# Kernel tuning notes

Measured on AMD Instinct MI355X. Metric: run time of the kernel, lower is better.

The kernel has to match this reference:

```python
import jax, jax.numpy as jnp
import numpy as np

N_NODES = 100000
N_EDGES = 600000
F_IN = 128
F_OUT = 128


def setup_inputs() -> dict:
    key = jax.random.key(0)
    ks = jax.random.split(key, 9)
    stdv = 1.0 / np.sqrt(F_OUT)
    return {
        "x": jax.random.normal(ks[0], (N_NODES, F_IN), dtype=jnp.float32),
        "weight": jax.random.uniform(ks[1], (F_IN, F_OUT), dtype=jnp.float32, minval=-stdv, maxval=stdv),
        "bias": jax.random.uniform(ks[2], (F_OUT,), dtype=jnp.float32, minval=-stdv, maxval=stdv),
        "vals0": jax.random.uniform(ks[3], (N_EDGES,), dtype=jnp.float32),
        "vals1": jax.random.uniform(ks[4], (N_EDGES,), dtype=jnp.float32),
        "rows0": jax.random.randint(ks[5], (N_EDGES,), 0, N_NODES, dtype=jnp.int32),
        "cols0": jax.random.randint(ks[6], (N_EDGES,), 0, N_NODES, dtype=jnp.int32),
        "rows1": jax.random.randint(ks[7], (N_EDGES,), 0, N_NODES, dtype=jnp.int32),
        "cols1": jax.random.randint(ks[8], (N_EDGES,), 0, N_NODES, dtype=jnp.int32),
    }


def _spmm(rows, cols, vals, dense, n):
    # COO sparse [n,n] @ dense [n,f]: gather source rows, scale, scatter-add to dest rows
    msgs = dense[cols] * vals[:, None]          # [E, f]
    return jax.ops.segment_sum(msgs, rows, num_segments=n)


def reference(x, weight, bias, vals0, vals1, rows0, cols0, rows1, cols1):
    n = x.shape[0]
    support = x @ weight                         # [N, F_OUT] dense GEMM
    out = _spmm(rows0, cols0, vals0, support, n) \
        + _spmm(rows1, cols1, vals1, support, n)
    return out + bias
```

## Files before the change

kernel.cpp:

```cpp
#include <hip/hip_runtime.h>


#define FDIM 128
#define EPB 2048

typedef __attribute__((ext_vector_type(8))) short short8;
typedef __attribute__((ext_vector_type(4))) float floatx4;

__device__ __forceinline__ unsigned short f32_to_bf16(float f) {
    unsigned int u = __float_as_uint(f);
    unsigned int r = u + 0x7fffu + ((u >> 16) & 1u);
    return (unsigned short)(r >> 16);
}

__device__ __forceinline__ float bf16_lo(unsigned int u) {
    return __uint_as_float((u & 0xffffu) << 16);
}
__device__ __forceinline__ float bf16_hi(unsigned int u) {
    return __uint_as_float(u & 0xffff0000u);
}

__global__ __launch_bounds__(256) void wt_conv(const float* __restrict__ w,
                                               unsigned short* __restrict__ wt) {
    int idx = blockIdx.x * 256 + threadIdx.x;
    int nn = idx >> 7, k = idx & 127;
    wt[idx] = f32_to_bf16(w[(size_t)k * FDIM + nn]);
}

__global__ __launch_bounds__(256) void gemm_mfma(const float* __restrict__ x,
                                                 const unsigned short* __restrict__ wt,
                                                 unsigned short* __restrict__ support,
                                                 int n) {
    __shared__ __align__(16) short As[64][136];
    __shared__ __align__(16) short Bs[128][136];
    const int tid = threadIdx.x;
    const int m0 = blockIdx.x * 64;

    #pragma unroll
    for (int i = 0; i < 8; ++i) {
        int idx = tid + i * 256;
        int r = idx >> 5, c4 = idx & 31;
        float4 v = make_float4(0.f, 0.f, 0.f, 0.f);
        if (m0 + r < n) v = *(const float4*)(x + (size_t)(m0 + r) * FDIM + c4 * 4);
        short4 s;
        s.x = (short)f32_to_bf16(v.x); s.y = (short)f32_to_bf16(v.y);
        s.z = (short)f32_to_bf16(v.z); s.w = (short)f32_to_bf16(v.w);
        *(short4*)&As[r][c4 * 4] = s;
    }
    #pragma unroll
    for (int i = 0; i < 8; ++i) {
        int idx = tid + i * 256;
        int r = idx >> 4, c8 = idx & 15;
        short8 v = *(const short8*)(wt + (size_t)r * FDIM + c8 * 8);
        *(short8*)&Bs[r][c8 * 8] = v;
    }
    __syncthreads();

    const int wv = tid >> 6;
    const int lane = tid & 63;
    const int quad = lane >> 4;
    const int lr = lane & 15;

    floatx4 acc[8];
    #pragma unroll
    for (int nt = 0; nt < 8; ++nt) acc[nt] = (floatx4)0.f;

    #pragma unroll
    for (int ks = 0; ks < 4; ++ks) {
        short8 a = *(const short8*)&As[wv * 16 + lr][ks * 32 + quad * 8];
        #pragma unroll
        for (int nt = 0; nt < 8; ++nt) {
            short8 b = *(const short8*)&Bs[nt * 16 + lr][ks * 32 + quad * 8];
            acc[nt] = __builtin_amdgcn_mfma_f32_16x16x32_bf16(a, b, acc[nt], 0, 0, 0);
        }
    }

    #pragma unroll
    for (int i = 0; i < 4; ++i) {
        int row = m0 + wv * 16 + quad * 4 + i;
        if (row < n) {
            #pragma unroll
            for (int nt = 0; nt < 8; ++nt)
                support[(size_t)row * FDIM + nt * 16 + lr] = f32_to_bf16(acc[nt][i]);
        }
    }
}

__global__ __launch_bounds__(256) void hist_rows(const int* __restrict__ rows0,
                                                 const int* __restrict__ rows1,
                                                 int* __restrict__ count,
                                                 int* __restrict__ rank, int E) {
    int gid = blockIdx.x * 256 + threadIdx.x;
    if (gid >= 2 * E) return;
    int r = (gid < E) ? rows0[gid] : rows1[gid - E];
    rank[gid] = atomicAdd(&count[r], 1);
}

__device__ __forceinline__ int block_incl_scan(int v, int tid, int* lds) {
    int lane = tid & 63, wv = tid >> 6;
    #pragma unroll
    for (int d = 1; d < 64; d <<= 1) {
        int y = __shfl_up(v, d);
        if (lane >= d) v += y;
    }
    if (lane == 63) lds[wv] = v;
    __syncthreads();
    if (wv == 0 && lane < 4) {
        int s = lds[lane];
        #pragma unroll
        for (int d = 1; d < 4; d <<= 1) {
            int y = __shfl_up(s, d);
            if (lane >= d) s += y;
        }
        lds[4 + lane] = s;
    }
    __syncthreads();
    int add = (wv > 0) ? lds[4 + wv - 1] : 0;
    return v + add;
}

__global__ __launch_bounds__(256) void block_sum(const int* __restrict__ count,
                                                 int* __restrict__ bsum, int n) {
    __shared__ int lds[8];
    int tid = threadIdx.x;
    int idx = blockIdx.x * 256 + tid;
    int v = (idx < n) ? count[idx] : 0;
    int inc = block_incl_scan(v, tid, lds);
    if (tid == 255) bsum[blockIdx.x] = inc;
}

__global__ __launch_bounds__(256) void scan_bsum(int* __restrict__ bsum, int nb) {
    __shared__ int lds[8];
    __shared__ int carry;
    int tid = threadIdx.x;
    if (tid == 0) carry = 0;
    __syncthreads();
    for (int base = 0; base < nb; base += 256) {
        int i = base + tid;
        int v = (i < nb) ? bsum[i] : 0;
        int inc = block_incl_scan(v, tid, lds);
        int c = carry;
        if (i < nb) bsum[i] = c + inc - v;
        __syncthreads();
        if (tid == 255) carry = c + inc;
        __syncthreads();
    }
}

__global__ __launch_bounds__(256) void write_ptr(const int* __restrict__ count,
                                                 const int* __restrict__ bscan,
                                                 int* __restrict__ rowptr,
                                                 int n, int total) {
    __shared__ int lds[8];
    int tid = threadIdx.x;
    int idx = blockIdx.x * 256 + tid;
    int v = (idx < n) ? count[idx] : 0;
    int inc = block_incl_scan(v, tid, lds);
    if (idx < n) rowptr[idx] = bscan[blockIdx.x] + inc - v;
    if (idx == 0) rowptr[n] = total;
}

__global__ __launch_bounds__(256) void scatter_part(
    const int* __restrict__ rows0, const int* __restrict__ cols0, const float* __restrict__ vals0,
    const int* __restrict__ rows1, const int* __restrict__ cols1, const float* __restrict__ vals1,
    const int* __restrict__ rank, const int* __restrict__ rowptr,
    int2* __restrict__ rec, int E, int nper) {
    const int p = blockIdx.x & 7;
    const int base = (blockIdx.x >> 3) * EPB;
    const int tid = threadIdx.x;
    #pragma unroll
    for (int it = 0; it < EPB / 256; ++it) {
        int gid = base + it * 256 + tid;
        if (gid < 2 * E) {
            int r = (gid < E) ? rows0[gid] : rows1[gid - E];
            if (r / nper == p) {
                int c; float v;
                if (gid < E) { c = cols0[gid]; v = vals0[gid]; }
                else         { int e = gid - E; c = cols1[e]; v = vals1[e]; }
                int pos = rowptr[r] + rank[gid];
                rec[pos] = make_int2(c, __float_as_int(v));
            }
        }
    }
}

__global__ __launch_bounds__(256) void pull_csr(const unsigned short* __restrict__ support,
                                                const int* __restrict__ rowptr,
                                                const int2* __restrict__ rec,
                                                const float* __restrict__ bias,
                                                float* __restrict__ out, int n) {
    int wid = (blockIdx.x * 256 + threadIdx.x) >> 6;
    int lane = threadIdx.x & 63;
    if (wid >= n) return;
    int beg = rowptr[wid], end = rowptr[wid + 1];
    float ax = 0.f, ay = 0.f;
    const char* sp = (const char*)support;
    const unsigned loff = (unsigned)lane << 2;

    for (int base = beg; base < end; base += 64) {
        int m = end - base; if (m > 64) m = 64;
        long long pk = 0;
        if (lane < m) pk = *(const long long*)&rec[base + lane];
        int j = 0;
        for (; j + 4 <= m; j += 4) {
            long long p0 = __shfl(pk, j);
            long long p1 = __shfl(pk, j + 1);
            long long p2 = __shfl(pk, j + 2);
            long long p3 = __shfl(pk, j + 3);
            unsigned u0 = *(const unsigned*)(sp + (((unsigned)p0) << 8) + loff);
            unsigned u1 = *(const unsigned*)(sp + (((unsigned)p1) << 8) + loff);
            unsigned u2 = *(const unsigned*)(sp + (((unsigned)p2) << 8) + loff);
            unsigned u3 = *(const unsigned*)(sp + (((unsigned)p3) << 8) + loff);
            float v0 = __int_as_float((int)(p0 >> 32));
            float v1 = __int_as_float((int)(p1 >> 32));
            float v2 = __int_as_float((int)(p2 >> 32));
            float v3 = __int_as_float((int)(p3 >> 32));
            ax += v0 * bf16_lo(u0); ay += v0 * bf16_hi(u0);
            ax += v1 * bf16_lo(u1); ay += v1 * bf16_hi(u1);
            ax += v2 * bf16_lo(u2); ay += v2 * bf16_hi(u2);
            ax += v3 * bf16_lo(u3); ay += v3 * bf16_hi(u3);
        }
        for (; j < m; ++j) {
            long long p = __shfl(pk, j);
            unsigned u = *(const unsigned*)(sp + (((unsigned)p) << 8) + loff);
            float v = __int_as_float((int)(p >> 32));
            ax += v * bf16_lo(u); ay += v * bf16_hi(u);
        }
    }
    float2 b = *(const float2*)(bias + lane * 2);
    *(float2*)(out + (size_t)wid * FDIM + lane * 2) = make_float2(ax + b.x, ay + b.y);
}

__global__ __launch_bounds__(256) void init_bias(const float* __restrict__ bias,
                                                 float* __restrict__ out, int n) {
    int idx = blockIdx.x * 256 + threadIdx.x;
    int total = n * (FDIM / 4);
    if (idx < total) {
        int j = (idx & (FDIM / 4 - 1)) * 4;
        float4 b = *(const float4*)(bias + j);
        *(float4*)(out + (size_t)idx * 4) = b;
    }
}

__global__ __launch_bounds__(256) void scatter_bf16(
    const unsigned short* __restrict__ support,
    const int* __restrict__ rows0, const int* __restrict__ cols0, const float* __restrict__ vals0,
    const int* __restrict__ rows1, const int* __restrict__ cols1, const float* __restrict__ vals1,
    float* __restrict__ out, int E) {
    int gid = blockIdx.x * 256 + threadIdx.x;
    int lane = gid & 63;
    int eg = gid >> 6;
    if (eg >= 2 * E) return;
    int r, c; float v;
    if (eg < E) { r = rows0[eg]; c = cols0[eg]; v = vals0[eg]; }
    else        { int e = eg - E; r = rows1[e]; c = cols1[e]; v = vals1[e]; }
    unsigned int u = *(const unsigned int*)(support + (size_t)c * FDIM + lane * 2);
    float sx = bf16_lo(u);
    float sy = bf16_hi(u);
    float* op = out + (size_t)r * FDIM + lane * 2;
    atomicAdd(op,     sx * v);
    atomicAdd(op + 1, sy * v);
}

static inline size_t align256(size_t v) { return (v + 255) & ~(size_t)255; }

extern "C" void kernel_launch(void* const* d_in, const int* in_sizes, int n_in,
                              void* d_out, int out_size, void* d_ws, size_t ws_size,
                              hipStream_t stream) {
    const float* x     = (const float*)d_in[0];
    const float* w     = (const float*)d_in[1];
    const float* bias  = (const float*)d_in[2];
    const float* vals0 = (const float*)d_in[3];
    const float* vals1 = (const float*)d_in[4];
    const int*   rows0 = (const int*)d_in[5];
    const int*   cols0 = (const int*)d_in[6];
    const int*   rows1 = (const int*)d_in[7];
    const int*   cols1 = (const int*)d_in[8];
    const int n = in_sizes[0] / FDIM;
    const int E = in_sizes[3];
    float* out = (float*)d_out;

    const int NB = (n + 255) / 256;

    size_t off = 0;
    unsigned short* support = (unsigned short*)((char*)d_ws + off);
    off = align256(off + (size_t)n * FDIM * 2);
    unsigned short* wt = (unsigned short*)((char*)d_ws + off);
    off = align256(off + (size_t)FDIM * FDIM * 2);
    int*  count  = (int*)((char*)d_ws + off);  off = align256(off + (size_t)n * 4);
    int*  rowptr = (int*)((char*)d_ws + off);  off = align256(off + (size_t)(n + 1) * 4);
    int*  rank   = (int*)((char*)d_ws + off);  off = align256(off + (size_t)2 * E * 4);
    int*  bsum   = (int*)((char*)d_ws + off);  off = align256(off + (size_t)NB * 4);
    int2* rec    = (int2*)((char*)d_ws + off); off = align256(off + (size_t)2 * E * 8);

    wt_conv<<<(FDIM * FDIM) / 256, 256, 0, stream>>>(w, wt);
    gemm_mfma<<<(n + 63) / 64, 256, 0, stream>>>(x, wt, support, n);

    if (off <= ws_size) {
        hipMemsetAsync(count, 0, (size_t)n * 4, stream);
        int eb = (2 * E + 255) / 256;
        hist_rows<<<eb, 256, 0, stream>>>(rows0, rows1, count, rank, E);
        block_sum<<<NB, 256, 0, stream>>>(count, bsum, n);
        scan_bsum<<<1, 256, 0, stream>>>(bsum, NB);
        write_ptr<<<NB, 256, 0, stream>>>(count, bsum, rowptr, n, 2 * E);
        int nper = (n + 7) / 8;
        int ntiles = (2 * E + EPB - 1) / EPB;
        scatter_part<<<ntiles * 8, 256, 0, stream>>>(rows0, cols0, vals0,
                                                     rows1, cols1, vals1,
                                                     rank, rowptr, rec, E, nper);
        pull_csr<<<(n + 3) / 4, 256, 0, stream>>>(support, rowptr, rec, bias, out, n);
    } else {
        int total4 = n * (FDIM / 4);
        init_bias<<<(total4 + 255) / 256, 256, 0, stream>>>(bias, out, n);
        long long tthreads = 2LL * E * 64;
        int blocks = (int)((tthreads + 255) / 256);
        scatter_bf16<<<blocks, 256, 0, stream>>>(support, rows0, cols0, vals0,
                                                 rows1, cols1, vals1, out, E);
    }
}
```

Before: 278.2 us.

## Replace three-pass scan with atomic-offset scan, precompute positions, register-resident GEMM

```diff
diff --git a/kernel.cpp b/kernel.cpp
--- a/kernel.cpp
+++ b/kernel.cpp
@@ -27,57 +27,54 @@
     wt[idx] = f32_to_bf16(w[(size_t)k * FDIM + nn]);
 }
 
-__global__ __launch_bounds__(256) void gemm_mfma(const float* __restrict__ x,
-                                                 const unsigned short* __restrict__ wt,
-                                                 unsigned short* __restrict__ support,
-                                                 int n) {
-    __shared__ __align__(16) short As[64][136];
-    __shared__ __align__(16) short Bs[128][136];
+__global__ __launch_bounds__(256) void gemm_reg(const float* __restrict__ x,
+                                                const unsigned short* __restrict__ wt,
+                                                unsigned short* __restrict__ support,
+                                                int n) {
     const int tid = threadIdx.x;
-    const int m0 = blockIdx.x * 64;
-
-    #pragma unroll
-    for (int i = 0; i < 8; ++i) {
-        int idx = tid + i * 256;
-        int r = idx >> 5, c4 = idx & 31;
-        float4 v = make_float4(0.f, 0.f, 0.f, 0.f);
-        if (m0 + r < n) v = *(const float4*)(x + (size_t)(m0 + r) * FDIM + c4 * 4);
-        short4 s;
-        s.x = (short)f32_to_bf16(v.x); s.y = (short)f32_to_bf16(v.y);
-        s.z = (short)f32_to_bf16(v.z); s.w = (short)f32_to_bf16(v.w);
-        *(short4*)&As[r][c4 * 4] = s;
-    }
-    #pragma unroll
-    for (int i = 0; i < 8; ++i) {
-        int idx = tid + i * 256;
-        int r = idx >> 4, c8 = idx & 15;
-        short8 v = *(const short8*)(wt + (size_t)r * FDIM + c8 * 8);
-        *(short8*)&Bs[r][c8 * 8] = v;
-    }
-    __syncthreads();
-
-    const int wv = tid >> 6;
-    const int lane = tid & 63;
-    const int quad = lane >> 4;
-    const int lr = lane & 15;
+    const int wv = tid >> 6, lane = tid & 63;
+    const int quad = lane >> 4, lr = lane & 15;
+    const int row0 = (blockIdx.x * 4 + wv) * 16;
+    if (row0 >= n) return;
+
+    short8 b[8][4];
+    #pragma unroll
+    for (int nt = 0; nt < 8; ++nt)
+        #pragma unroll
+        for (int ks = 0; ks < 4; ++ks)
+            b[nt][ks] = *(const short8*)(wt + (size_t)(nt * 16 + lr) * FDIM + ks * 32 + quad * 8);
 
     floatx4 acc[8];
     #pragma unroll
     for (int nt = 0; nt < 8; ++nt) acc[nt] = (floatx4)0.f;
 
+    const int arow = row0 + lr;
+    const bool rowok = arow < n;
+    const float* xr = x + (size_t)arow * FDIM;
+
+    float4 f[8];
     #pragma unroll
     for (int ks = 0; ks < 4; ++ks) {
-        short8 a = *(const short8*)&As[wv * 16 + lr][ks * 32 + quad * 8];
+        f[2 * ks]     = rowok ? *(const float4*)(xr + ks * 32 + quad * 8)     : make_float4(0.f,0.f,0.f,0.f);
+        f[2 * ks + 1] = rowok ? *(const float4*)(xr + ks * 32 + quad * 8 + 4) : make_float4(0.f,0.f,0.f,0.f);
+    }
+
+    #pragma unroll
+    for (int ks = 0; ks < 4; ++ks) {
+        float4 lo = f[2 * ks], hi = f[2 * ks + 1];
+        short8 a;
+        a[0] = (short)f32_to_bf16(lo.x); a[1] = (short)f32_to_bf16(lo.y);
+        a[2] = (short)f32_to_bf16(lo.z); a[3] = (short)f32_to_bf16(lo.w);
+        a[4] = (short)f32_to_bf16(hi.x); a[5] = (short)f32_to_bf16(hi.y);
+        a[6] = (short)f32_to_bf16(hi.z); a[7] = (short)f32_to_bf16(hi.w);
         #pragma unroll
-        for (int nt = 0; nt < 8; ++nt) {
-            short8 b = *(const short8*)&Bs[nt * 16 + lr][ks * 32 + quad * 8];
-            acc[nt] = __builtin_amdgcn_mfma_f32_16x16x32_bf16(a, b, acc[nt], 0, 0, 0);
-        }
+        for (int nt = 0; nt < 8; ++nt)
+            acc[nt] = __builtin_amdgcn_mfma_f32_16x16x32_bf16(a, b[nt][ks], acc[nt], 0, 0, 0);
     }
 
     #pragma unroll
     for (int i = 0; i < 4; ++i) {
-        int row = m0 + wv * 16 + quad * 4 + i;
+        int row = row0 + quad * 4 + i;
         if (row < n) {
             #pragma unroll
             for (int nt = 0; nt < 8; ++nt)
@@ -119,52 +116,36 @@
     return v + add;
 }
 
-__global__ __launch_bounds__(256) void block_sum(const int* __restrict__ count,
-                                                 int* __restrict__ bsum, int n) {
+__global__ __launch_bounds__(256) void rowptr_scan(const int* __restrict__ count,
+                                                   int* __restrict__ rowptr,
+                                                   int* __restrict__ gcur, int n) {
     __shared__ int lds[8];
+    __shared__ int base;
     int tid = threadIdx.x;
     int idx = blockIdx.x * 256 + tid;
     int v = (idx < n) ? count[idx] : 0;
     int inc = block_incl_scan(v, tid, lds);
-    if (tid == 255) bsum[blockIdx.x] = inc;
-}
-
-__global__ __launch_bounds__(256) void scan_bsum(int* __restrict__ bsum, int nb) {
-    __shared__ int lds[8];
-    __shared__ int carry;
-    int tid = threadIdx.x;
-    if (tid == 0) carry = 0;
+    if (tid == 255) base = atomicAdd(gcur, inc);
     __syncthreads();
-    for (int base = 0; base < nb; base += 256) {
-        int i = base + tid;
-        int v = (i < nb) ? bsum[i] : 0;
-        int inc = block_incl_scan(v, tid, lds);
-        int c = carry;
-        if (i < nb) bsum[i] = c + inc - v;
-        __syncthreads();
-        if (tid == 255) carry = c + inc;
-        __syncthreads();
-    }
-}
-
-__global__ __launch_bounds__(256) void write_ptr(const int* __restrict__ count,
-                                                 const int* __restrict__ bscan,
-                                                 int* __restrict__ rowptr,
-                                                 int n, int total) {
-    __shared__ int lds[8];
-    int tid = threadIdx.x;
-    int idx = blockIdx.x * 256 + tid;
-    int v = (idx < n) ? count[idx] : 0;
-    int inc = block_incl_scan(v, tid, lds);
-    if (idx < n) rowptr[idx] = bscan[blockIdx.x] + inc - v;
-    if (idx == 0) rowptr[n] = total;
-}
-
-__global__ __launch_bounds__(256) void scatter_part(
-    const int* __restrict__ rows0, const int* __restrict__ cols0, const float* __restrict__ vals0,
-    const int* __restrict__ rows1, const int* __restrict__ cols1, const float* __restrict__ vals1,
-    const int* __restrict__ rank, const int* __restrict__ rowptr,
-    int2* __restrict__ rec, int E, int nper) {
+    if (idx < n) rowptr[idx] = base + inc - v;
+}
+
+__global__ __launch_bounds__(256) void compute_pos(const int* __restrict__ rows0,
+                                                   const int* __restrict__ rows1,
+                                                   const int* __restrict__ rank,
+                                                   const int* __restrict__ rowptr,
+                                                   int* __restrict__ pos, int E) {
+    int gid = blockIdx.x * 256 + threadIdx.x;
+    if (gid >= 2 * E) return;
+    int r = (gid < E) ? rows0[gid] : rows1[gid - E];
+    pos[gid] = rowptr[r] + rank[gid];
+}
+
+__global__ __launch_bounds__(256) void scatter_pos(
+    const int* __restrict__ cols0, const float* __restrict__ vals0,
+    const int* __restrict__ cols1, const float* __restrict__ vals1,
+    const int* __restrict__ pos,
+    int2* __restrict__ rec, int E, int psize) {
     const int p = blockIdx.x & 7;
     const int base = (blockIdx.x >> 3) * EPB;
     const int tid = threadIdx.x;
@@ -172,13 +153,12 @@
     for (int it = 0; it < EPB / 256; ++it) {
         int gid = base + it * 256 + tid;
         if (gid < 2 * E) {
-            int r = (gid < E) ? rows0[gid] : rows1[gid - E];
-            if (r / nper == p) {
+            int pv = pos[gid];
+            if (pv / psize == p) {
                 int c; float v;
                 if (gid < E) { c = cols0[gid]; v = vals0[gid]; }
                 else         { int e = gid - E; c = cols1[e]; v = vals1[e]; }
-                int pos = rowptr[r] + rank[gid];
-                rec[pos] = make_int2(c, __float_as_int(v));
+                rec[pv] = make_int2(c, __float_as_int(v));
             }
         }
     }
@@ -186,13 +166,15 @@
 
 __global__ __launch_bounds__(256) void pull_csr(const unsigned short* __restrict__ support,
                                                 const int* __restrict__ rowptr,
+                                                const int* __restrict__ count,
                                                 const int2* __restrict__ rec,
                                                 const float* __restrict__ bias,
                                                 float* __restrict__ out, int n) {
     int wid = (blockIdx.x * 256 + threadIdx.x) >> 6;
     int lane = threadIdx.x & 63;
     if (wid >= n) return;
-    int beg = rowptr[wid], end = rowptr[wid + 1];
+    int beg = rowptr[wid];
+    int end = beg + count[wid];
     float ax = 0.f, ay = 0.f;
     const char* sp = (const char*)support;
     const unsigned loff = (unsigned)lane << 2;
@@ -202,6 +184,40 @@
         long long pk = 0;
         if (lane < m) pk = *(const long long*)&rec[base + lane];
         int j = 0;
+        for (; j + 8 <= m; j += 8) {
+            long long p0 = __shfl(pk, j);
+            long long p1 = __shfl(pk, j + 1);
+            long long p2 = __shfl(pk, j + 2);
+            long long p3 = __shfl(pk, j + 3);
+            long long p4 = __shfl(pk, j + 4);
+            long long p5 = __shfl(pk, j + 5);
+            long long p6 = __shfl(pk, j + 6);
+            long long p7 = __shfl(pk, j + 7);
+            unsigned u0 = *(const unsigned*)(sp + (((unsigned)p0) << 8) + loff);
+            unsigned u1 = *(const unsigned*)(sp + (((unsigned)p1) << 8) + loff);
+            unsigned u2 = *(const unsigned*)(sp + (((unsigned)p2) << 8) + loff);
+            unsigned u3 = *(const unsigned*)(sp + (((unsigned)p3) << 8) + loff);
+            unsigned u4 = *(const unsigned*)(sp + (((unsigned)p4) << 8) + loff);
+            unsigned u5 = *(const unsigned*)(sp + (((unsigned)p5) << 8) + loff);
+            unsigned u6 = *(const unsigned*)(sp + (((unsigned)p6) << 8) + loff);
+            unsigned u7 = *(const unsigned*)(sp + (((unsigned)p7) << 8) + loff);
+            float v0 = __int_as_float((int)(p0 >> 32));
+            float v1 = __int_as_float((int)(p1 >> 32));
+            float v2 = __int_as_float((int)(p2 >> 32));
+            float v3 = __int_as_float((int)(p3 >> 32));
+            float v4 = __int_as_float((int)(p4 >> 32));
+            float v5 = __int_as_float((int)(p5 >> 32));
+            float v6 = __int_as_float((int)(p6 >> 32));
+            float v7 = __int_as_float((int)(p7 >> 32));
+            ax += v0 * bf16_lo(u0); ay += v0 * bf16_hi(u0);
+            ax += v1 * bf16_lo(u1); ay += v1 * bf16_hi(u1);
+            ax += v2 * bf16_lo(u2); ay += v2 * bf16_hi(u2);
+            ax += v3 * bf16_lo(u3); ay += v3 * bf16_hi(u3);
+            ax += v4 * bf16_lo(u4); ay += v4 * bf16_hi(u4);
+            ax += v5 * bf16_lo(u5); ay += v5 * bf16_hi(u5);
+            ax += v6 * bf16_lo(u6); ay += v6 * bf16_hi(u6);
+            ax += v7 * bf16_lo(u7); ay += v7 * bf16_hi(u7);
+        }
         for (; j + 4 <= m; j += 4) {
             long long p0 = __shfl(pk, j);
             long long p1 = __shfl(pk, j + 1);
@@ -287,28 +303,29 @@
     off = align256(off + (size_t)n * FDIM * 2);
     unsigned short* wt = (unsigned short*)((char*)d_ws + off);
     off = align256(off + (size_t)FDIM * FDIM * 2);
+    size_t count_off = off;
     int*  count  = (int*)((char*)d_ws + off);  off = align256(off + (size_t)n * 4);
-    int*  rowptr = (int*)((char*)d_ws + off);  off = align256(off + (size_t)(n + 1) * 4);
+    int*  gcur   = (int*)((char*)d_ws + off);  off = align256(off + 4);
+    size_t zero_bytes = off - count_off;
+    int*  rowptr = (int*)((char*)d_ws + off);  off = align256(off + (size_t)n * 4);
     int*  rank   = (int*)((char*)d_ws + off);  off = align256(off + (size_t)2 * E * 4);
-    int*  bsum   = (int*)((char*)d_ws + off);  off = align256(off + (size_t)NB * 4);
+    int*  pos    = (int*)((char*)d_ws + off);  off = align256(off + (size_t)2 * E * 4);
     int2* rec    = (int2*)((char*)d_ws + off); off = align256(off + (size_t)2 * E * 8);
 
     wt_conv<<<(FDIM * FDIM) / 256, 256, 0, stream>>>(w, wt);
-    gemm_mfma<<<(n + 63) / 64, 256, 0, stream>>>(x, wt, support, n);
+    gemm_reg<<<(n + 63) / 64, 256, 0, stream>>>(x, wt, support, n);
 
     if (off <= ws_size) {
-        hipMemsetAsync(count, 0, (size_t)n * 4, stream);
+        hipMemsetAsync((char*)d_ws + count_off, 0, zero_bytes, stream);
         int eb = (2 * E + 255) / 256;
         hist_rows<<<eb, 256, 0, stream>>>(rows0, rows1, count, rank, E);
-        block_sum<<<NB, 256, 0, stream>>>(count, bsum, n);
-        scan_bsum<<<1, 256, 0, stream>>>(bsum, NB);
-        write_ptr<<<NB, 256, 0, stream>>>(count, bsum, rowptr, n, 2 * E);
-        int nper = (n + 7) / 8;
+        rowptr_scan<<<NB, 256, 0, stream>>>(count, rowptr, gcur, n);
+        compute_pos<<<eb, 256, 0, stream>>>(rows0, rows1, rank, rowptr, pos, E);
+        int psize = (2 * E + 7) / 8;
         int ntiles = (2 * E + EPB - 1) / EPB;
-        scatter_part<<<ntiles * 8, 256, 0, stream>>>(rows0, cols0, vals0,
-                                                     rows1, cols1, vals1,
-                                                     rank, rowptr, rec, E, nper);
-        pull_csr<<<(n + 3) / 4, 256, 0, stream>>>(support, rowptr, rec, bias, out, n);
+        scatter_pos<<<ntiles * 8, 256, 0, stream>>>(cols0, vals0, cols1, vals1,
+                                                    pos, rec, E, psize);
+        pull_csr<<<(n + 3) / 4, 256, 0, stream>>>(support, rowptr, count, rec, bias, out, n);
     } else {
         int total4 = n * (FDIM / 4);
         init_bias<<<(total4 + 255) / 256, 256, 0, stream>>>(bias, out, n);
```

Measured after the change: 291.7 us. 1.05x slower.
